# Kernel tuning notes

Hardware: AMD Instinct MI355X
Metric: run time of the kernel (lower is better)

## Reference

```python
import jax, jax.numpy as jnp
import numpy as np

# Kobayashi dendrite-growth parameters (init_params values from the repo)
TAU = 3e-4
EPSILONB = 0.01
KAPPA = 1.8
DELTA = 0.02
ANISO = 6.0
ALPHA = 0.9
GAMMA = 10.0
TEQ = 1.0
THETA0 = 0.2
PIX = 4.0 * np.arctan(1.0)  # pi
DX = 0.03
DY = 0.03
DT = 1e-4

B, H, W = 4, 2048, 2048


def lap(u, dx, dy):
    # 5-point Laplacian, periodic boundaries. x = last axis, y = second-to-last.
    return ((jnp.roll(u, -1, -1) + jnp.roll(u, 1, -1) - 2.0 * u) / (dx * dx)
            + (jnp.roll(u, -1, -2) + jnp.roll(u, 1, -2) - 2.0 * u) / (dy * dy))


def grad(u, axis_name, d):
    ax = -1 if axis_name == 'x' else -2
    return (jnp.roll(u, -1, ax) - jnp.roll(u, 1, ax)) / (2.0 * d)


def setup_inputs() -> dict:
    key = jax.random.key(0)
    k1, k2 = jax.random.split(key)
    phi = jax.random.uniform(k1, (B, H, W), dtype=jnp.float32)
    tempr = jax.random.uniform(k2, (B, H, W), dtype=jnp.float32)
    return {"phi": phi, "tempr": tempr}


def reference(phi, tempr):
    lap_phi = lap(phi, DX, DY)
    lap_tempr = lap(tempr, DX, DY)
    phidx = grad(phi, 'x', DX)
    phidy = grad(phi, 'y', DY)
    theta = jnp.arctan2(phidy, phidx)
    epsilon = EPSILONB * (1.0 + DELTA * jnp.cos(ANISO * (theta - THETA0)))
    epsilon_deriv = -EPSILONB * ANISO * DELTA * jnp.sin(ANISO * (theta - THETA0))
    prod_mat1 = epsilon * epsilon_deriv * phidx
    prod_mat2 = -epsilon * epsilon_deriv * phidy
    term1 = grad(prod_mat1, 'y', DY)
    term2 = grad(prod_mat2, 'x', DX)
    m = ALPHA / PIX * jnp.arctan(GAMMA * (TEQ - tempr))
    dphi_dt = DT / TAU * (term1 + term2 + epsilon ** 2 * lap_phi
                          + phi * (1.0 - phi) * (phi - 0.5 + m))
    phi_new = phi + dphi_dt
    tempr_new = tempr + DT * lap_tempr + KAPPA * dphi_dt
    return (phi_new, tempr_new)
```

## Files before the change

### kernel.cpp

```cpp
#include <hip/hip_runtime.h>
#include <math.h>


#define Bz 4
#define Hd 2048
#define Wd 2048
#define SH 32
#define WPB 4

#define INVD2   1111.11111111111f
#define K1c     277.777777777778f
#define DT_TAU  0.333333333333333f
#define DTc     1e-4f
#define KAPPAc  1.8f
#define EPSB    0.01f
#define DELTAc  0.02f
#define ANISOc  6.0f
#define A_PI    0.2864788975654116f
#define GAMMAc  10.0f
#define TEQc    1.0f
#define C6T0    0.3623577544766736f
#define S6T0    0.9320390859672263f
#define PI_2    1.5707963267948966f

__device__ __forceinline__ void prodc(float dx, float dy,
                                      float& p1, float& p2, float& e2)
{
    float dx2 = dx * dx;
    float r2  = fmaf(dy, dy, dx2);
    float cn  = fmaf(-dy, dy, dx2);
    float irr = __builtin_amdgcn_rcpf(fmaxf(r2, 1e-20f));
    float c2  = cn * irr;
    float s2  = 2.0f * dx * dy * irr;
    float c6  = c2 * fmaf(4.0f, c2 * c2, -3.0f);
    float s6  = s2 * fmaf(-4.0f, s2 * s2, 3.0f);
    float cosA = fmaf(c6, C6T0, s6 * S6T0);
    float sinA = fmaf(s6, C6T0, -c6 * S6T0);
    float eps  = fmaf(EPSB * DELTAc, cosA, EPSB);
    float ee   = eps * (-EPSB * ANISOc * DELTAc) * sinA;
    p1 = ee * dx;
    p2 = -ee * dy;
    e2 = eps * eps;
}

__device__ __forceinline__ float atan_fast(float g) {
    float r  = __builtin_amdgcn_rcpf(g);
    float a  = fminf(g, r);
    float a2 = a * a;
    float p  = a * fmaf(a2, fmaf(a2, 0.079331f, -0.288679f), 0.995354f);
    return (g <= 1.0f) ? p : PI_2 - p;
}

__global__ __launch_bounds__(256) void dendrite_step(
    const float* __restrict__ phi, const float* __restrict__ tempr,
    float* __restrict__ out_phi, float* __restrict__ out_tempr)
{
    const int tid  = threadIdx.x;
    const int lane = tid & 63;
    const int wv   = tid >> 6;
    const int x0   = blockIdx.x * 64;
    const int y0   = blockIdx.y * (WPB * SH) + wv * SH;
    const int base = blockIdx.z * (Hd * Wd);
    const int gx   = x0 + lane;

    const bool eL = (lane == 0);
    const bool eR = (lane == 63);
    const bool eE = eL || eR;
    const int hxc = eL ? ((x0 - 2) & (Wd - 1)) : ((x0 + 64) & (Wd - 1));
    const int thx = eL ? ((x0 - 1) & (Wd - 1)) : ((x0 + 64) & (Wd - 1));

    auto prow = [&](const float* a, int r) {
        return a + base + ((y0 + r) & (Hd - 1)) * Wd;
    };

    float pc_m2 = prow(phi, -2)[gx];
    float pc_m1 = prow(phi, -1)[gx];
    float pc_0  = prow(phi,  0)[gx];
    float pc_p1 = prow(phi,  1)[gx];
    float pc_p2 = prow(phi,  2)[gx];
    float tm = prow(tempr, -1)[gx];
    float tc = prow(tempr,  0)[gx];
    float tn = prow(tempr,  1)[gx];

    float2 Hmm = make_float2(0.f, 0.f), Hm = Hmm, Hc = Hmm, Hp = Hmm;
    float tH_c = 0.0f;
    if (eE) {
        Hmm = *(const float2*)(prow(phi, -1) + hxc);
        Hm  = *(const float2*)(prow(phi,  0) + hxc);
        Hc  = *(const float2*)(prow(phi,  1) + hxc);
        Hp  = *(const float2*)(prow(phi,  2) + hxc);
        tH_c = prow(tempr, 0)[thx];
    }

    float plm = __shfl_up(pc_m1, 1), prm = __shfl_down(pc_m1, 1);
    float plc = __shfl_up(pc_0, 1),  prc = __shfl_down(pc_0, 1);
    if (eL) { plm = Hmm.y; plc = Hm.y; }
    if (eR) { prm = Hmm.x; prc = Hm.x; }
    float tlc = __shfl_up(tc, 1), trc = __shfl_down(tc, 1);
    if (eL) tlc = tH_c;
    if (eR) trc = tH_c;

    float p1m, p1c, p2c, e2c, du0, du1;
    prodc(prm - plm, pc_0 - pc_m2, p1m, du0, du1);
    prodc(prc - plc, pc_p1 - pc_m1, p1c, p2c, e2c);

    float p2h_c = 0.0f;
    if (eE) {
        float dxh = eL ? (pc_0 - Hm.x) : (Hm.y - pc_0);
        float mp  = eL ? Hc.y  : Hc.x;
        float mmv = eL ? Hmm.y : Hmm.x;
        float a, c_;
        prodc(dxh, mp - mmv, a, p2h_c, c_);
        (void)a; (void)c_;
    }

    const int omask = Hd * Wd - 1;
    int oP  = ((y0 + 3) & (Hd - 1)) * Wd;
    int oT  = ((y0 + 2) & (Hd - 1)) * Wd;
    int oTH = ((y0 + 1) & (Hd - 1)) * Wd;
    int gout = base + y0 * Wd + gx;

    #pragma unroll 4
    for (int k = 0; k < SH; ++k) {
        float ph_new = phi[base + oP + gx];
        float t_new  = tempr[base + oT + gx];
        float2 H_new = make_float2(0.f, 0.f);
        float tH_n = 0.0f;
        if (eE) {
            H_new = *(const float2*)(phi + base + oP + hxc);
            tH_n  = tempr[base + oTH + thx];
        }

        float pl1 = __shfl_up(pc_p1, 1), pr1 = __shfl_down(pc_p1, 1);
        if (eL) pl1 = Hc.y;
        if (eR) pr1 = Hc.x;
        float p1p, p2n, e2n;
        prodc(pr1 - pl1, pc_p2 - pc_0, p1p, p2n, e2n);

        float p2h_n = 0.0f;
        if (eE) {
            float dxh = eL ? (pc_p1 - Hc.x) : (Hc.y - pc_p1);
            float mp  = eL ? Hp.y : Hp.x;
            float mmv = eL ? Hm.y : Hm.x;
            float a, c_;
            prodc(dxh, mp - mmv, a, p2h_n, c_);
            (void)a; (void)c_;
        }

        float tl_n = __shfl_up(tn, 1), tr_n = __shfl_down(tn, 1);
        if (eL) tl_n = tH_n;
        if (eR) tr_n = tH_n;

        float p2l = __shfl_up(p2c, 1), p2r = __shfl_down(p2c, 1);
        if (eL) p2l = p2h_c;
        if (eR) p2r = p2h_c;

        float t12  = (p1p - p1m + p2r - p2l) * K1c;
        float lapp = (plc + prc + pc_m1 + pc_p1 - 4.0f * pc_0) * INVD2;
        float lapt = (tlc + trc + tm + tn - 4.0f * tc) * INVD2;
        float mval = A_PI * atan_fast(GAMMAc * (TEQc - tc));
        float dphi = DT_TAU * (t12 + e2c * lapp
                       + pc_0 * (1.0f - pc_0) * (pc_0 - 0.5f + mval));
        out_phi[gout]   = pc_0 + dphi;
        out_tempr[gout] = fmaf(KAPPAc, dphi, fmaf(DTc, lapt, tc));

        pc_m1 = pc_0; pc_0 = pc_p1; pc_p1 = pc_p2; pc_p2 = ph_new;
        plc = pl1; prc = pr1;
        p1m = p1c; p1c = p1p;
        p2c = p2n; e2c = e2n; p2h_c = p2h_n;
        tm = tc; tc = tn; tn = t_new;
        tlc = tl_n; trc = tr_n;
        Hm = Hc; Hc = Hp; Hp = H_new;

        oP  = (oP  + Wd) & omask;
        oT  = (oT  + Wd) & omask;
        oTH = (oTH + Wd) & omask;
        gout += Wd;
    }
}

extern "C" void kernel_launch(void* const* d_in, const int* in_sizes, int n_in,
                              void* d_out, int out_size, void* d_ws, size_t ws_size,
                              hipStream_t stream) {
    const float* phi = (const float*)d_in[0];
    const float* tempr = (const float*)d_in[1];
    float* out_phi = (float*)d_out;
    float* out_tempr = out_phi + (size_t)Bz * Hd * Wd;

    dim3 grid(Wd / 64, Hd / (WPB * SH), Bz);
    dendrite_step<<<grid, 256, 0, stream>>>(phi, tempr, out_phi, out_tempr);
}
```

Baseline: 250.6 us.

## Process four columns per thread with float4 loads and stores in stencil

Each lane now handles four adjacent x-columns using float4 vector loads and stores, so a wave covers 256 columns and fewer shuffles are needed per output. The column strip per wave is halved to keep the grid size up, a min-blocks-per-CU hint of 4 is added, and the last-iteration prefetch is skipped. The aim is fewer memory instructions and less shuffle overhead per element. In exchange, register pressure rises, halo overhead per block grows in relative terms, and occupancy may drop.

```diff
diff --git a/kernel.cpp b/kernel.cpp
--- a/kernel.cpp
+++ b/kernel.cpp
@@ -5,7 +5,7 @@
 #define Bz 4
 #define Hd 2048
 #define Wd 2048
-#define SH 32
+#define SH 16
 #define WPB 4
 
 #define INVD2   1111.11111111111f
@@ -51,36 +51,52 @@
     return (g <= 1.0f) ? p : PI_2 - p;
 }
 
-__global__ __launch_bounds__(256) void dendrite_step(
+__device__ __forceinline__ void cellout(
+    float pm, float pc, float pp, float pl, float pr,
+    float p1p_, float p1m_, float p2l_, float p2r_, float e2_,
+    float tm_, float tc_, float tn_, float tl_, float tr_,
+    float& op, float& ot)
+{
+    float t12  = (p1p_ - p1m_ + p2r_ - p2l_) * K1c;
+    float lapp = (pl + pr + pm + pp - 4.0f * pc) * INVD2;
+    float lapt = (tl_ + tr_ + tm_ + tn_ - 4.0f * tc_) * INVD2;
+    float mval = A_PI * atan_fast(GAMMAc * (TEQc - tc_));
+    float dphi = DT_TAU * (t12 + e2_ * lapp
+                   + pc * (1.0f - pc) * (pc - 0.5f + mval));
+    op = pc + dphi;
+    ot = fmaf(KAPPAc, dphi, fmaf(DTc, lapt, tc_));
+}
+
+__global__ __launch_bounds__(256, 4) void dendrite_step(
     const float* __restrict__ phi, const float* __restrict__ tempr,
     float* __restrict__ out_phi, float* __restrict__ out_tempr)
 {
     const int tid  = threadIdx.x;
     const int lane = tid & 63;
     const int wv   = tid >> 6;
-    const int x0   = blockIdx.x * 64;
+    const int x0   = blockIdx.x * 256;
     const int y0   = blockIdx.y * (WPB * SH) + wv * SH;
     const int base = blockIdx.z * (Hd * Wd);
-    const int gx   = x0 + lane;
+    const int gx   = x0 + 4 * lane;
 
     const bool eL = (lane == 0);
     const bool eR = (lane == 63);
     const bool eE = eL || eR;
-    const int hxc = eL ? ((x0 - 2) & (Wd - 1)) : ((x0 + 64) & (Wd - 1));
-    const int thx = eL ? ((x0 - 1) & (Wd - 1)) : ((x0 + 64) & (Wd - 1));
+    const int hxc = eL ? ((x0 - 2) & (Wd - 1)) : ((x0 + 256) & (Wd - 1));
+    const int thx = eL ? ((x0 - 1) & (Wd - 1)) : ((x0 + 256) & (Wd - 1));
 
     auto prow = [&](const float* a, int r) {
         return a + base + ((y0 + r) & (Hd - 1)) * Wd;
     };
 
-    float pc_m2 = prow(phi, -2)[gx];
-    float pc_m1 = prow(phi, -1)[gx];
-    float pc_0  = prow(phi,  0)[gx];
-    float pc_p1 = prow(phi,  1)[gx];
-    float pc_p2 = prow(phi,  2)[gx];
-    float tm = prow(tempr, -1)[gx];
-    float tc = prow(tempr,  0)[gx];
-    float tn = prow(tempr,  1)[gx];
+    float4 P0 = *(const float4*)(prow(phi, -2) + gx);
+    float4 P1 = *(const float4*)(prow(phi, -1) + gx);
+    float4 P2 = *(const float4*)(prow(phi,  0) + gx);
+    float4 P3 = *(const float4*)(prow(phi,  1) + gx);
+    float4 P4 = *(const float4*)(prow(phi,  2) + gx);
+    float4 T0 = *(const float4*)(prow(tempr, -1) + gx);
+    float4 T1 = *(const float4*)(prow(tempr,  0) + gx);
+    float4 T2 = *(const float4*)(prow(tempr,  1) + gx);
 
     float2 Hmm = make_float2(0.f, 0.f), Hm = Hmm, Hc = Hmm, Hp = Hmm;
     float tH_c = 0.0f;
@@ -92,21 +108,32 @@
         tH_c = prow(tempr, 0)[thx];
     }
 
-    float plm = __shfl_up(pc_m1, 1), prm = __shfl_down(pc_m1, 1);
-    float plc = __shfl_up(pc_0, 1),  prc = __shfl_down(pc_0, 1);
-    if (eL) { plm = Hmm.y; plc = Hm.y; }
-    if (eR) { prm = Hmm.x; prc = Hm.x; }
-    float tlc = __shfl_up(tc, 1), trc = __shfl_down(tc, 1);
+    float plm = __shfl_up(P1.w, 1), prm = __shfl_down(P1.x, 1);
+    if (eL) plm = Hmm.y;
+    if (eR) prm = Hmm.x;
+    float plc = __shfl_up(P2.w, 1), prc = __shfl_down(P2.x, 1);
+    if (eL) plc = Hm.y;
+    if (eR) prc = Hm.x;
+    float tlc = __shfl_up(T1.w, 1), trc = __shfl_down(T1.x, 1);
     if (eL) tlc = tH_c;
     if (eR) trc = tH_c;
 
-    float p1m, p1c, p2c, e2c, du0, du1;
-    prodc(prm - plm, pc_0 - pc_m2, p1m, du0, du1);
-    prodc(prc - plc, pc_p1 - pc_m1, p1c, p2c, e2c);
+    float4 p1m, p1c, p2c, e2c;
+    {
+        float d0, d1;
+        prodc(P1.y - plm,  P2.x - P0.x, p1m.x, d0, d1);
+        prodc(P1.z - P1.x, P2.y - P0.y, p1m.y, d0, d1);
+        prodc(P1.w - P1.y, P2.z - P0.z, p1m.z, d0, d1);
+        prodc(prm  - P1.z, P2.w - P0.w, p1m.w, d0, d1);
+    }
+    prodc(P2.y - plc,  P3.x - P1.x, p1c.x, p2c.x, e2c.x);
+    prodc(P2.z - P2.x, P3.y - P1.y, p1c.y, p2c.y, e2c.y);
+    prodc(P2.w - P2.y, P3.z - P1.z, p1c.z, p2c.z, e2c.z);
+    prodc(prc  - P2.z, P3.w - P1.w, p1c.w, p2c.w, e2c.w);
 
     float p2h_c = 0.0f;
     if (eE) {
-        float dxh = eL ? (pc_0 - Hm.x) : (Hm.y - pc_0);
+        float dxh = eL ? (P2.x - Hm.x) : (Hm.y - P2.w);
         float mp  = eL ? Hc.y  : Hc.x;
         float mmv = eL ? Hmm.y : Hmm.x;
         float a, c_;
@@ -122,24 +149,34 @@
 
     #pragma unroll 4
     for (int k = 0; k < SH; ++k) {
-        float ph_new = phi[base + oP + gx];
-        float t_new  = tempr[base + oT + gx];
-        float2 H_new = make_float2(0.f, 0.f);
-        float tH_n = 0.0f;
-        if (eE) {
-            H_new = *(const float2*)(phi + base + oP + hxc);
-            tH_n  = tempr[base + oTH + thx];
+        float4 Pn = make_float4(0.f, 0.f, 0.f, 0.f);
+        float4 Tn = Pn;
+        float2 Hn = make_float2(0.f, 0.f);
+        float tHn = 0.0f;
+        if (k < SH - 1) {
+            Pn = *(const float4*)(phi + base + oP + gx);
+            Tn = *(const float4*)(tempr + base + oT + gx);
+            if (eE) {
+                Hn  = *(const float2*)(phi + base + oP + hxc);
+                tHn = tempr[base + oTH + thx];
+            }
+        } else if (eE) {
+            tHn = tempr[base + oTH + thx];
         }
 
-        float pl1 = __shfl_up(pc_p1, 1), pr1 = __shfl_down(pc_p1, 1);
+        float pl1 = __shfl_up(P3.w, 1), pr1 = __shfl_down(P3.x, 1);
         if (eL) pl1 = Hc.y;
         if (eR) pr1 = Hc.x;
-        float p1p, p2n, e2n;
-        prodc(pr1 - pl1, pc_p2 - pc_0, p1p, p2n, e2n);
+
+        float4 p1p, p2n, e2n;
+        prodc(P3.y - pl1,  P4.x - P2.x, p1p.x, p2n.x, e2n.x);
+        prodc(P3.z - P3.x, P4.y - P2.y, p1p.y, p2n.y, e2n.y);
+        prodc(P3.w - P3.y, P4.z - P2.z, p1p.z, p2n.z, e2n.z);
+        prodc(pr1  - P3.z, P4.w - P2.w, p1p.w, p2n.w, e2n.w);
 
         float p2h_n = 0.0f;
         if (eE) {
-            float dxh = eL ? (pc_p1 - Hc.x) : (Hc.y - pc_p1);
+            float dxh = eL ? (P3.x - Hc.x) : (Hc.y - P3.w);
             float mp  = eL ? Hp.y : Hp.x;
             float mmv = eL ? Hm.y : Hm.x;
             float a, c_;
@@ -147,30 +184,34 @@
             (void)a; (void)c_;
         }
 
-        float tl_n = __shfl_up(tn, 1), tr_n = __shfl_down(tn, 1);
-        if (eL) tl_n = tH_n;
-        if (eR) tr_n = tH_n;
-
-        float p2l = __shfl_up(p2c, 1), p2r = __shfl_down(p2c, 1);
+        float tl_n = __shfl_up(T2.w, 1), tr_n = __shfl_down(T2.x, 1);
+        if (eL) tl_n = tHn;
+        if (eR) tr_n = tHn;
+
+        float p2l = __shfl_up(p2c.w, 1), p2r = __shfl_down(p2c.x, 1);
         if (eL) p2l = p2h_c;
         if (eR) p2r = p2h_c;
 
-        float t12  = (p1p - p1m + p2r - p2l) * K1c;
-        float lapp = (plc + prc + pc_m1 + pc_p1 - 4.0f * pc_0) * INVD2;
-        float lapt = (tlc + trc + tm + tn - 4.0f * tc) * INVD2;
-        float mval = A_PI * atan_fast(GAMMAc * (TEQc - tc));
-        float dphi = DT_TAU * (t12 + e2c * lapp
-                       + pc_0 * (1.0f - pc_0) * (pc_0 - 0.5f + mval));
-        out_phi[gout]   = pc_0 + dphi;
-        out_tempr[gout] = fmaf(KAPPAc, dphi, fmaf(DTc, lapt, tc));
-
-        pc_m1 = pc_0; pc_0 = pc_p1; pc_p1 = pc_p2; pc_p2 = ph_new;
+        float4 OPv, OTv;
+        cellout(P1.x, P2.x, P3.x, plc,  P2.y, p1p.x, p1m.x, p2l,   p2c.y,
+                e2c.x, T0.x, T1.x, T2.x, tlc,  T1.y, OPv.x, OTv.x);
+        cellout(P1.y, P2.y, P3.y, P2.x, P2.z, p1p.y, p1m.y, p2c.x, p2c.z,
+                e2c.y, T0.y, T1.y, T2.y, T1.x, T1.z, OPv.y, OTv.y);
+        cellout(P1.z, P2.z, P3.z, P2.y, P2.w, p1p.z, p1m.z, p2c.y, p2c.w,
+                e2c.z, T0.z, T1.z, T2.z, T1.y, T1.w, OPv.z, OTv.z);
+        cellout(P1.w, P2.w, P3.w, P2.z, prc,  p1p.w, p1m.w, p2c.z, p2r,
+                e2c.w, T0.w, T1.w, T2.w, T1.z, trc,  OPv.w, OTv.w);
+
+        *(float4*)(out_phi + gout)   = OPv;
+        *(float4*)(out_tempr + gout) = OTv;
+
+        P0 = P1; P1 = P2; P2 = P3; P3 = P4; P4 = Pn;
         plc = pl1; prc = pr1;
         p1m = p1c; p1c = p1p;
         p2c = p2n; e2c = e2n; p2h_c = p2h_n;
-        tm = tc; tc = tn; tn = t_new;
+        T0 = T1; T1 = T2; T2 = Tn;
         tlc = tl_n; trc = tr_n;
-        Hm = Hc; Hc = Hp; Hp = H_new;
+        Hm = Hc; Hc = Hp; Hp = Hn;
 
         oP  = (oP  + Wd) & omask;
         oT  = (oT  + Wd) & omask;
@@ -187,6 +228,6 @@
     float* out_phi = (float*)d_out;
     float* out_tempr = out_phi + (size_t)Bz * Hd * Wd;
 
-    dim3 grid(Wd / 64, Hd / (WPB * SH), Bz);
+    dim3 grid(Wd / 256, Hd / (WPB * SH), Bz);
     dendrite_step<<<grid, 256, 0, stream>>>(phi, tempr, out_phi, out_tempr);
 }
```

Result: no change. 251.4 us (+0.3%).
